# Kernel tuning notes

Hardware: AMD Instinct MI355X
Metric: run time of the kernel (lower is better)

## Reference

```python
import jax, jax.numpy as jnp
import numpy as np

RRELU_SLOPE = (1.0 / 8.0 + 1.0 / 3.0) / 2.0  # F.rrelu eval mode
N_ENT, N_REL2, H, E, B, T = 20000, 460, 128, 400000, 1024, 8


def _lin(x, W, b):
    return x @ W.T + b  # torch nn.Linear convention


def _gru_cell(x, h, w_ih, w_hh, b_ih, b_hh):
    gi = x @ w_ih.T + b_ih
    gh = h @ w_hh.T + b_hh
    i_r, i_z, i_n = jnp.split(gi, 3, axis=1)
    h_r, h_z, h_n = jnp.split(gh, 3, axis=1)
    r = jax.nn.sigmoid(i_r + h_r)
    z = jax.nn.sigmoid(i_z + h_z)
    n = jnp.tanh(i_n + r * h_n)
    return (1.0 - z) * n + z * h


def setup_inputs() -> dict:
    key = jax.random.key(0)
    ks = jax.random.split(key, 24)
    s = 0.02
    inp = {
        'ent_emb': jax.random.normal(ks[0], (N_ENT, H), jnp.float32),
        'rel_emb': jax.random.normal(ks[1], (N_REL2, H), jnp.float32),
        'weight_neighbor': jax.random.normal(ks[2], (H, H), jnp.float32) * s,
        'loop_weight': jax.random.normal(ks[3], (H, H), jnp.float32) * s,
        'evolve_loop_weight': jax.random.normal(ks[4], (H, H), jnp.float32) * s,
        'w_ih': jax.random.normal(ks[5], (3 * H, H), jnp.float32) * s,
        'w_hh': jax.random.normal(ks[6], (3 * H, H), jnp.float32) * s,
        'b_ih': jnp.zeros((3 * H,), jnp.float32),
        'b_hh': jnp.zeros((3 * H,), jnp.float32),
        'W_map1': jax.random.normal(ks[7], (2 * H, H), jnp.float32) * s,
        'b_map1': jnp.zeros((2 * H,), jnp.float32),
        'W_map2': jax.random.normal(ks[8], (H, 2 * H), jnp.float32) * s,
        'b_map2': jnp.zeros((H,), jnp.float32),
        'W_h1': jax.random.normal(ks[9], (H, H), jnp.float32) * s,
        'b_h1': jnp.zeros((H,), jnp.float32),
        'W_h2': jax.random.normal(ks[10], (H, H), jnp.float32) * s,
        'b_h2': jnp.zeros((H,), jnp.float32),
        'W_align': jax.random.normal(ks[11], (H, H), jnp.float32) * s,
        'b_align': jnp.zeros((H,), jnp.float32),
        'W_attn': jax.random.normal(ks[12], (H, H), jnp.float32) * s,
        'b_attn': jnp.zeros((H,), jnp.float32),
    }
    u = jax.random.uniform(ks[13], (B, T * N_REL2), jnp.float32)
    mask = jax.random.uniform(ks[14], (B, T * N_REL2)) > 0.7  # sparse history
    inp['partial_embeding'] = u * mask
    inp['edge_src'] = jax.random.randint(ks[15], (E,), 0, N_ENT, jnp.int32)
    inp['edge_dst'] = jax.random.randint(ks[16], (E,), 0, N_ENT, jnp.int32)
    inp['edge_type'] = jax.random.randint(ks[17], (E,), 0, N_REL2, jnp.int32)
    sub = jax.random.randint(ks[18], (B,), 0, N_ENT, jnp.int32)
    rel = jax.random.randint(ks[19], (B,), 0, N_REL2, jnp.int32)
    obj = jax.random.randint(ks[20], (B,), 0, N_ENT, jnp.int32)
    inp['triples'] = jnp.stack([sub, rel, obj], axis=1)
    return inp


def reference(ent_emb, rel_emb, weight_neighbor, loop_weight, evolve_loop_weight,
              w_ih, w_hh, b_ih, b_hh, W_map1, b_map1, W_map2, b_map2,
              W_h1, b_h1, W_h2, b_h2, W_align, b_align, W_attn, b_attn,
              partial_embeding, edge_src, edge_dst, edge_type, triples):
    # ---- UnionRGCNLayer: gather-transform-scatter ----
    h = ent_emb
    msg = (h[edge_src] + rel_emb[edge_type]) @ weight_neighbor          # [E, H]
    agg = jax.ops.segment_sum(msg, edge_dst, num_segments=N_ENT)        # [N, H]
    deg = jax.ops.segment_sum(jnp.ones((edge_dst.shape[0],), h.dtype), edge_dst,
                              num_segments=N_ENT)
    norm = jnp.where(deg > 0, 1.0 / jnp.where(deg > 0, deg, 1.0), 0.0)[:, None]
    loop = jnp.where((deg > 0)[:, None], h @ loop_weight, h @ evolve_loop_weight)
    x = agg * norm + loop
    pre_emb = jnp.where(x >= 0, x, x * RRELU_SLOPE)                     # rrelu (eval)

    # ---- PathPredictor.forward_back ----
    mapped_rel = _lin(_lin(rel_emb, W_map1, b_map1), W_map2, b_map2)    # [2R, H]
    q_rel = mapped_rel[triples[:, 1]]                                   # [B, H]
    A = _lin(q_rel, W_attn, b_attn) @ mapped_rel.T                      # [B, 2R]
    hist = partial_embeding.reshape(B, T, N_REL2).transpose(1, 0, 2)    # [T, B, 2R]

    def step(gh, cur):
        attn = cur * A
        attn = jax.nn.softmax(jnp.where(attn == 0, -1e9, attn), axis=1)
        rel_path = attn @ mapped_rel                                    # [B, H]
        return _gru_cell(rel_path, gh, w_ih, w_hh, b_ih, b_hh), None

    gru_hidden, _ = jax.lax.scan(step, jnp.zeros((B, H), pre_emb.dtype), hist)
    predicted_hist = 0.1 * _lin(_lin(q_rel, W_h1, b_h1), W_h2, b_h2) + q_rel
    match_loss = jnp.mean((predicted_hist - gru_hidden) ** 2)

    # ---- forward_forth, distmult scoring ----
    gh2 = _gru_cell(q_rel, predicted_hist, w_ih, w_hh, b_ih, b_hh)      # [B, H]
    sub_emb = pre_emb[triples[:, 0]]
    aligned_all = _lin(pre_emb, W_align, b_align)                       # [N, H]
    score_ = (_lin(sub_emb, W_align, b_align) * gh2) @ aligned_all.T    # [B, N]
    score = jax.nn.sigmoid(score_)
    # BCE(score, one_hot(obj)) without materializing labels:
    logp = jax.nn.log_sigmoid(score_)
    log1mp = jax.nn.log_sigmoid(-score_)
    total = -jnp.sum(log1mp)
    rows = jnp.arange(B)
    total = total + jnp.sum(log1mp[rows, triples[:, 2]] - logp[rows, triples[:, 2]])
    path_loss = total / (B * N_ENT)
    return score, match_loss, path_loss
```

## Files before the change

kernel.cpp:

```cpp
#include <hip/hip_runtime.h>

typedef unsigned short u16;
typedef unsigned int u32;
typedef __attribute__((ext_vector_type(8))) short bf8v;
typedef __attribute__((ext_vector_type(4))) float f4v;

#define RRELU_SLOPE 0.22916666667f

__device__ inline float bf2f(u16 u){ unsigned int i = ((unsigned int)u) << 16; float f; __builtin_memcpy(&f, &i, 4); return f; }
__device__ inline u16 f2bf(float f){ unsigned int i; __builtin_memcpy(&i, &f, 4); unsigned int r = (i + 0x7fffu + ((i >> 16) & 1u)) >> 16; return (u16)r; }
__device__ inline float frcp(float x){ return __builtin_amdgcn_rcpf(x); }
__device__ inline float fsigm(float x){ return frcp(1.f + __expf(-x)); }
__device__ inline float ftanh(float x){ return 2.f * frcp(1.f + __expf(-2.f * x)) - 1.f; }

__global__ __launch_bounds__(256) void prep_k(
    const float* __restrict__ Wn, const float* __restrict__ Wl, const float* __restrict__ We,
    const float* __restrict__ wih, const float* __restrict__ whh,
    const float* __restrict__ m1, const float* __restrict__ m2,
    const float* __restrict__ h1, const float* __restrict__ h2,
    const float* __restrict__ attn, const float* __restrict__ alg, const float* __restrict__ rel,
    const float* __restrict__ ent, const float* __restrict__ bat, const float* __restrict__ bh1,
    const float* __restrict__ bm1, const float* __restrict__ bm2,
    const int* __restrict__ edst, int E,
    u16* __restrict__ Bcat, u16* __restrict__ wihb, u16* __restrict__ whhb,
    u16* __restrict__ m1b, u16* __restrict__ m2b, u16* __restrict__ h1b, u16* __restrict__ h2b,
    u16* __restrict__ attnb, u16* __restrict__ algb, u16* __restrict__ relb,
    u16* __restrict__ entb, float* __restrict__ bias2,
    u16* __restrict__ wcb, float* __restrict__ bcombf, int* __restrict__ hist)
{
    int id = blockIdx.x * 256 + threadIdx.x;
    if (id < 49152) {
        int n = id / 384, k = id % 384;
        float v = (k < 128) ? Wn[k*128 + n] : (k < 256 ? Wl[(k-128)*128 + n] : We[(k-256)*128 + n]);
        Bcat[id] = f2bf(v); return;
    }
    id -= 49152;
    if (id < 49152) { wihb[id] = f2bf(wih[id]); return; } id -= 49152;
    if (id < 49152) { whhb[id] = f2bf(whh[id]); return; } id -= 49152;
    if (id < 32768) { m1b[id]  = f2bf(m1[id]);  return; } id -= 32768;
    if (id < 32768) { m2b[id]  = f2bf(m2[id]);  return; } id -= 32768;
    if (id < 16384) { h1b[id]  = f2bf(h1[id]);  return; } id -= 16384;
    if (id < 16384) { h2b[id]  = f2bf(h2[id]);  return; } id -= 16384;
    if (id < 16384) { attnb[id]= f2bf(attn[id]);return; } id -= 16384;
    if (id < 16384) { algb[id] = f2bf(alg[id]); return; } id -= 16384;
    if (id < 58880) { relb[id] = f2bf(rel[id]); return; } id -= 58880;
    if (id < 2560000) { entb[id] = f2bf(ent[id]); return; } id -= 2560000;
    if (id < 256) { bias2[id] = (id < 128) ? bat[id] : bh1[id - 128]; return; } id -= 256;
    if (id < 16384) {
        int n = id >> 7, j = id & 127;
        const float* w2r = m2 + n * 256;
        float s = 0.f;
        for (int k = 0; k < 256; ++k) s += w2r[k] * m1[k*128 + j];
        wcb[id] = f2bf(s); return;
    } id -= 16384;
    if (id < 128) {
        const float* w2r = m2 + id * 256;
        float s = bm2[id];
        for (int k = 0; k < 256; ++k) s += w2r[k] * bm1[k];
        bcombf[id] = s; return;
    } id -= 128;
    if (id < E) atomicAdd(&hist[edst[id]], 1);
}

__global__ __launch_bounds__(1024) void scan_k(
    const int* __restrict__ hist, int* __restrict__ starts, int* __restrict__ cursor)
{
    __shared__ int part[1024];
    int t = threadIdx.x;
    int base = t * 20;
    int s = 0;
    for (int j = 0; j < 20; ++j) { int idx = base + j; if (idx < 20000) s += hist[idx]; }
    part[t] = s;
    __syncthreads();
    for (int off = 1; off < 1024; off <<= 1) {
        int v = (t >= off) ? part[t - off] : 0;
        __syncthreads();
        part[t] += v;
        __syncthreads();
    }
    int run = (t > 0) ? part[t - 1] : 0;
    for (int j = 0; j < 20; ++j) {
        int idx = base + j;
        if (idx < 20000) { starts[idx] = run; cursor[idx] = run; run += hist[idx]; }
    }
    if (t == 1023) starts[20000] = run;
}

__global__ __launch_bounds__(256) void scmap_k(
    const int* __restrict__ src, const int* __restrict__ dst, const int* __restrict__ typ,
    int* __restrict__ cursor, int2* __restrict__ spack, int E, int eb,
    const u16* __restrict__ relb, const u16* __restrict__ wcb, const float* __restrict__ bcombf,
    u16* __restrict__ mapb, u16* __restrict__ mapT)
{
    int tid = threadIdx.x;
    if ((int)blockIdx.x < eb) {
        int e = blockIdx.x * 256 + tid;
        if (e >= E) return;
        int d = dst[e];
        int p = atomicAdd(&cursor[d], 1);
        spack[p] = make_int2(src[e], typ[e]);
        return;
    }
    int wave = tid >> 6, lane = tid & 63;
    int ln = lane & 15, q = lane >> 4;
    int base = (blockIdx.x - eb) * 64 + wave * 16;
    int arow = base + ln; if (arow > 459) arow = 459;
    const u16* Ap = relb + arow * 128;
    f4v acc[8] = {};
    for (int kc = 0; kc < 128; kc += 32) {
        bf8v af = *(const bf8v*)(Ap + kc + q*8);
#pragma unroll
        for (int nt = 0; nt < 8; ++nt) {
            bf8v bv = *(const bf8v*)(wcb + (nt*16 + ln)*128 + kc + q*8);
            acc[nt] = __builtin_amdgcn_mfma_f32_16x16x32_bf16(af, bv, acc[nt], 0, 0, 0);
        }
    }
#pragma unroll
    for (int nt = 0; nt < 8; ++nt) {
        int n = nt*16 + ln;
        float bv = bcombf[n];
#pragma unroll
        for (int r = 0; r < 4; ++r) {
            int m = base + q*4 + r;
            if (m < 460) {
                u16 hv = f2bf(acc[nt][r] + bv);
                mapb[m*128 + n] = hv;
                mapT[n*480 + m] = hv;
            }
        }
    }
}

__global__ __launch_bounds__(256) void agg_k(
    const int2* __restrict__ spack, const int* __restrict__ starts,
    const u32* __restrict__ hb, const u32* __restrict__ rb, u32* __restrict__ Acat32)
{
    int tid = threadIdx.x;
    int wave = tid >> 6, lane = tid & 63;
    int i = blockIdx.x * 4 + wave;
    int s0 = starts[i], s1 = starts[i + 1];
    float sx = 0.f, sy = 0.f;
    int e = s0;
    for (; e + 4 <= s1; e += 4) {
        int2 st0 = spack[e], st1 = spack[e+1], st2 = spack[e+2], st3 = spack[e+3];
        u32 a0 = hb[(long)st0.x * 64 + lane]; u32 r0 = rb[(long)st0.y * 64 + lane];
        u32 a1 = hb[(long)st1.x * 64 + lane]; u32 r1 = rb[(long)st1.y * 64 + lane];
        u32 a2 = hb[(long)st2.x * 64 + lane]; u32 r2 = rb[(long)st2.y * 64 + lane];
        u32 a3 = hb[(long)st3.x * 64 + lane]; u32 r3 = rb[(long)st3.y * 64 + lane];
        sx += bf2f((u16)(a0 & 0xffff)) + bf2f((u16)(r0 & 0xffff));
        sy += bf2f((u16)(a0 >> 16))    + bf2f((u16)(r0 >> 16));
        sx += bf2f((u16)(a1 & 0xffff)) + bf2f((u16)(r1 & 0xffff));
        sy += bf2f((u16)(a1 >> 16))    + bf2f((u16)(r1 >> 16));
        sx += bf2f((u16)(a2 & 0xffff)) + bf2f((u16)(r2 & 0xffff));
        sy += bf2f((u16)(a2 >> 16))    + bf2f((u16)(r2 >> 16));
        sx += bf2f((u16)(a3 & 0xffff)) + bf2f((u16)(r3 & 0xffff));
        sy += bf2f((u16)(a3 >> 16))    + bf2f((u16)(r3 >> 16));
    }
    for (; e < s1; ++e) {
        int2 st = spack[e];
        u32 a = hb[(long)st.x * 64 + lane];
        u32 r = rb[(long)st.y * 64 + lane];
        sx += bf2f((u16)(a & 0xffff)) + bf2f((u16)(r & 0xffff));
        sy += bf2f((u16)(a >> 16))    + bf2f((u16)(r >> 16));
    }
    bool has = s1 > s0;
    float nrm = has ? frcp((float)(s1 - s0)) : 0.f;
    u32 hv = hb[(long)i * 64 + lane];
    u32 agg = (u32)f2bf(sx * nrm) | ((u32)f2bf(sy * nrm) << 16);
    long o = (long)i * 192 + lane;
    Acat32[o]       = agg;
    Acat32[o + 64]  = has ? hv : 0u;
    Acat32[o + 128] = has ? 0u : hv;
}

__global__ __launch_bounds__(256) void prealnq_k(
    const u16* __restrict__ acat, const u16* __restrict__ bcat,
    const u16* __restrict__ alb, const float* __restrict__ bal,
    u16* __restrict__ preb, u16* __restrict__ alnb,
    const u16* __restrict__ mapb, const int* __restrict__ trip,
    const u16* __restrict__ atb, const float* __restrict__ bias2,
    const u16* __restrict__ h2b, const float* __restrict__ bh2,
    u16* __restrict__ atq, float* __restrict__ pred, u16* __restrict__ X)
{
    __shared__ u16 lds[4][16][136];
    int tid = threadIdx.x;
    int wave = tid >> 6, lane = tid & 63;
    int ln = lane & 15, q = lane >> 4;
    if (blockIdx.x < 313) {
        int bm = blockIdx.x * 64 + wave * 16;
        int am = bm + ln; if (am > 19999) am = 19999;
        const u16* Ap = acat + (long)am * 384;
        f4v acc[8] = {};
        for (int kc = 0; kc < 384; kc += 32) {
            bf8v af = *(const bf8v*)(Ap + kc + q*8);
#pragma unroll
            for (int nt = 0; nt < 8; ++nt) {
                bf8v bv = *(const bf8v*)(bcat + (nt*16 + ln)*384 + kc + q*8);
                acc[nt] = __builtin_amdgcn_mfma_f32_16x16x32_bf16(af, bv, acc[nt], 0, 0, 0);
            }
        }
#pragma unroll
        for (int nt = 0; nt < 8; ++nt) {
            int n = nt*16 + ln;
#pragma unroll
            for (int r = 0; r < 4; ++r) {
                int m = bm + q*4 + r;
                float v = acc[nt][r];
                v = (v >= 0.f) ? v : v * RRELU_SLOPE;
                u16 hv = f2bf(v);
                lds[wave][q*4 + r][n] = hv;
                if (m < 20000) preb[(long)m*128 + n] = hv;
            }
        }
        f4v acc2[8] = {};
        for (int kc = 0; kc < 128; kc += 32) {
            bf8v af = *(const bf8v*)&lds[wave][ln][kc + q*8];
#pragma unroll
            for (int nt = 0; nt < 8; ++nt) {
                bf8v bv = *(const bf8v*)(alb + (nt*16 + ln)*128 + kc + q*8);
                acc2[nt] = __builtin_amdgcn_mfma_f32_16x16x32_bf16(af, bv, acc2[nt], 0, 0, 0);
            }
        }
#pragma unroll
        for (int nt = 0; nt < 8; ++nt) {
            int n = nt*16 + ln;
            float bv = bal[n];
#pragma unroll
            for (int r = 0; r < 4; ++r) {
                int m = bm + q*4 + r;
                if (m < 20000) alnb[(long)m*128 + n] = f2bf(acc2[nt][r] + bv);
            }
        }
        return;
    }
    int base = (blockIdx.x - 313) * 64 + wave * 16;
    int ar = trip[(base + ln)*3 + 1];
    const u16* Ap = mapb + ar * 128;
    int rm_[4];
#pragma unroll
    for (int r = 0; r < 4; ++r) rm_[r] = trip[(base + q*4 + r)*3 + 1];
    f4v acc1[16] = {};
    for (int kc = 0; kc < 128; kc += 32) {
        bf8v af = *(const bf8v*)(Ap + kc + q*8);
#pragma unroll
        for (int nt = 0; nt < 16; ++nt) {
            bf8v bv = *(const bf8v*)(atb + (nt*16 + ln)*128 + kc + q*8);
            acc1[nt] = __builtin_amdgcn_mfma_f32_16x16x32_bf16(af, bv, acc1[nt], 0, 0, 0);
        }
    }
#pragma unroll
    for (int nt = 0; nt < 16; ++nt) {
        int n = nt*16 + ln;
        float bv = bias2[n];
#pragma unroll
        for (int r = 0; r < 4; ++r) {
            int m = base + q*4 + r;
            float x = acc1[nt][r] + bv;
            if (nt < 8) {
                atq[m*128 + n] = f2bf(x);
                X[(long)(8192 + m)*128 + n] = mapb[rm_[r]*128 + n];
            } else lds[wave][q*4 + r][n - 128] = f2bf(x);
        }
    }
    f4v acc2[8] = {};
    for (int kc = 0; kc < 128; kc += 32) {
        bf8v af = *(const bf8v*)&lds[wave][ln][kc + q*8];
#pragma unroll
        for (int nt = 0; nt < 8; ++nt) {
            bf8v bv = *(const bf8v*)(h2b + (nt*16 + ln)*128 + kc + q*8);
            acc2[nt] = __builtin_amdgcn_mfma_f32_16x16x32_bf16(af, bv, acc2[nt], 0, 0, 0);
        }
    }
#pragma unroll
    for (int nt = 0; nt < 8; ++nt) {
        int n = nt*16 + ln;
        float bv = bh2[n];
#pragma unroll
        for (int r = 0; r < 4; ++r) {
            int m = base + q*4 + r;
            pred[(long)m*128 + n] = 0.1f * (acc2[nt][r] + bv) + bf2f(mapb[rm_[r]*128 + n]);
        }
    }
}

__global__ __launch_bounds__(256) void smrp_k(
    const u16* __restrict__ atq, const u16* __restrict__ mapb,
    const float* __restrict__ part, const u16* __restrict__ mapT, u16* __restrict__ X)
{
    __shared__ u16 xls[32][488];
    __shared__ float asl[4][464];
    int tid = threadIdx.x;
    int wave = tid >> 6, lane = tid & 63;
    int ln = lane & 15, q = lane >> 4;
    int b0 = blockIdx.x * 4;
    {
        const u16* Ap = atq + (long)(b0 + (ln & 3)) * 128;
        bf8v af[4];
#pragma unroll
        for (int kc = 0; kc < 4; ++kc) af[kc] = *(const bf8v*)(Ap + kc*32 + q*8);
        for (int nt = wave; nt < 29; nt += 4) {
            int brow = nt*16 + ln; if (brow > 459) brow = 459;
            f4v acc = {};
#pragma unroll
            for (int kc = 0; kc < 4; ++kc) {
                bf8v bv = *(const bf8v*)(mapb + (long)brow*128 + kc*32 + q*8);
                acc = __builtin_amdgcn_mfma_f32_16x16x32_bf16(af[kc], bv, acc, 0, 0, 0);
            }
            if (q == 0) {
                int n = nt*16 + ln;
                if (n < 460) {
#pragma unroll
                    for (int r = 0; r < 4; ++r) asl[r][n] = acc[r];
                }
            }
        }
    }
    __syncthreads();
    for (int j = 0; j < 8; ++j) {
        int rl = wave*8 + j;
        int t = rl >> 2, db = rl & 3;
        const float* crow = part + (long)(b0 + db)*3680 + t*460;
        float v[8], e[8];
        float m = -1e30f;
#pragma unroll
        for (int i = 0; i < 8; ++i) {
            int r = i*64 + lane;
            if (r < 460) {
                float x = crow[r] * asl[db][r];
                x = (x == 0.f) ? -1e9f : x;
                v[i] = x; m = fmaxf(m, x);
            } else v[i] = -1e30f;
        }
#pragma unroll
        for (int off = 32; off; off >>= 1) m = fmaxf(m, __shfl_xor(m, off));
        float sum = 0.f;
#pragma unroll
        for (int i = 0; i < 8; ++i) {
            int r = i*64 + lane;
            e[i] = 0.f;
            if (r < 460) { e[i] = __expf(v[i] - m); sum += e[i]; }
        }
#pragma unroll
        for (int off = 32; off; off >>= 1) sum += __shfl_xor(sum, off);
        float inv = frcp(sum);
#pragma unroll
        for (int i = 0; i < 8; ++i) {
            int r = i*64 + lane;
            if (r < 460)      xls[rl][r] = f2bf(e[i] * inv);
            else if (r < 488) xls[rl][r] = 0;
        }
    }
    __syncthreads();
    f4v acc[2][2] = {};
    for (int kc = 0; kc < 480; kc += 32) {
        bf8v a[2], bfr[2];
#pragma unroll
        for (int mt = 0; mt < 2; ++mt)
            a[mt] = *(const bf8v*)&xls[mt*16 + ln][kc + q*8];
#pragma unroll
        for (int nt = 0; nt < 2; ++nt)
            bfr[nt] = *(const bf8v*)(mapT + (wave*32 + nt*16 + ln)*480 + kc + q*8);
#pragma unroll
        for (int mt = 0; mt < 2; ++mt)
#pragma unroll
            for (int nt = 0; nt < 2; ++nt)
                acc[mt][nt] = __builtin_amdgcn_mfma_f32_16x16x32_bf16(a[mt], bfr[nt], acc[mt][nt], 0, 0, 0);
    }
#pragma unroll
    for (int mt = 0; mt < 2; ++mt)
#pragma unroll
    for (int nt = 0; nt < 2; ++nt) {
        int n = wave*32 + nt*16 + ln;
#pragma unroll
        for (int r = 0; r < 4; ++r) {
            int rl = mt*16 + q*4 + r;
            long m = (long)(rl >> 2)*1024 + b0 + (rl & 3);
            X[m*128 + n] = f2bf(acc[mt][nt][r]);
        }
    }
}

__global__ __launch_bounds__(256, 1) void gru_k(
    const u16* __restrict__ X, const u16* __restrict__ wihb, const float* __restrict__ bih,
    const u16* __restrict__ whhb, const float* __restrict__ bhh,
    const float* __restrict__ pred,
    const u16* __restrict__ preb, const u16* __restrict__ alb, const float* __restrict__ bal,
    const u16* __restrict__ AL, const int* __restrict__ trip,
    u16* __restrict__ V, float* __restrict__ accp)
{
    __shared__ u16  hbf[16][136];
    __shared__ float hf [4][128];
    __shared__ float ghl[4][388];
    __shared__ float gil[4][388];
    __shared__ float sll[4][132];
    __shared__ float redm[4], redo[4];
    int tid = threadIdx.x;
    int wave = tid >> 6, lane = tid & 63;
    int ln = lane & 15, q = lane >> 4;
    int bb = blockIdx.x * 4;
    for (int i = tid; i < 16*136; i += 256) hbf[i/136][i%136] = 0;
    for (int i = tid; i < 4*128; i += 256) hf[i>>7][i&127] = 0.f;
    bf8v bfrag[6][4], wfrag[6][4];
#pragma unroll
    for (int nt = 0; nt < 6; ++nt)
#pragma unroll
        for (int kc = 0; kc < 4; ++kc) {
            bfrag[nt][kc] = *(const bf8v*)(whhb + (long)(wave*96 + nt*16 + ln)*128 + kc*32 + q*8);
            wfrag[nt][kc] = *(const bf8v*)(wihb + (long)(wave*96 + nt*16 + ln)*128 + kc*32 + q*8);
        }
    {
        const u16* Pp = preb + (long)trip[(bb + (ln & 3))*3 + 0] * 128;
        f4v sacc[2] = {};
#pragma unroll
        for (int kc = 0; kc < 4; ++kc) {
            bf8v pf = *(const bf8v*)(Pp + kc*32 + q*8);
#pragma unroll
            for (int nt = 0; nt < 2; ++nt) {
                bf8v bv = *(const bf8v*)(alb + (long)(wave*32 + nt*16 + ln)*128 + kc*32 + q*8);
                sacc[nt] = __builtin_amdgcn_mfma_f32_16x16x32_bf16(pf, bv, sacc[nt], 0, 0, 0);
            }
        }
        if (q == 0) {
#pragma unroll
            for (int nt = 0; nt < 2; ++nt) {
                int n = wave*32 + nt*16 + ln;
                float bv = bal[n];
#pragma unroll
                for (int r = 0; r < 4; ++r) sll[r][n] = sacc[nt][r] + bv;
            }
        }
    }
    int k = tid & 127;
    float cr = bih[k] + bhh[k];
    float cz = bih[128 + k] + bhh[128 + k];
    float bin_ = bih[256 + k], bhn = bhh[256 + k];
    __syncthreads();
    float msum = 0.f, osum = 0.f;
    for (int t = 0; t <= 8; ++t) {
        float pv[2];
#pragma unroll
        for (int it = 0; it < 2; ++it) {
            int m = it*2 + (tid >> 7);
            pv[it] = (t >= 7) ? pred[(long)(bb + m)*128 + k] : 0.f;
        }
        if (t == 8) {
#pragma unroll
            for (int it = 0; it < 2; ++it) {
                int m = it*2 + (tid >> 7);
                hf[m][k] = pv[it]; hbf[m][k] = f2bf(pv[it]);
            }
            __syncthreads();
        }
        long xr0 = (t < 8) ? ((long)t*1024 + bb) : (long)(8192 + bb);
        const u16* Xp = X + (xr0 + (ln & 3))*128;
        f4v gacc[6] = {};
        f4v acc[6] = {};
#pragma unroll
        for (int kc = 0; kc < 4; ++kc) {
            bf8v xf = *(const bf8v*)(Xp + kc*32 + q*8);
            bf8v af = *(const bf8v*)&hbf[ln][kc*32 + q*8];
#pragma unroll
            for (int nt = 0; nt < 6; ++nt) {
                gacc[nt] = __builtin_amdgcn_mfma_f32_16x16x32_bf16(xf, wfrag[nt][kc], gacc[nt], 0, 0, 0);
                acc[nt]  = __builtin_amdgcn_mfma_f32_16x16x32_bf16(af, bfrag[nt][kc], acc[nt],  0, 0, 0);
            }
        }
        if (q == 0) {
#pragma unroll
            for (int nt = 0; nt < 6; ++nt)
#pragma unroll
                for (int r = 0; r < 4; ++r) {
                    ghl[r][wave*96 + nt*16 + ln] = acc[nt][r];
                    gil[r][wave*96 + nt*16 + ln] = gacc[nt][r];
                }
        }
        __syncthreads();
#pragma unroll
        for (int it = 0; it < 2; ++it) {
            int m = it*2 + (tid >> 7);
            float rr = fsigm(gil[m][k] + ghl[m][k] + cr);
            float zz = fsigm(gil[m][128 + k] + ghl[m][128 + k] + cz);
            float nn = ftanh(gil[m][256 + k] + bin_ + rr * (ghl[m][256 + k] + bhn));
            float hn = (1.f - zz) * nn + zz * hf[m][k];
            if (t == 7) { float d = pv[it] - hn; msum += d*d; }
            if (t == 8) {
                u16 vb = f2bf(sll[m][k] * hn);
                V[(long)(bb + m)*128 + k] = vb;
                int obj = trip[(bb + m)*3 + 2];
                osum += bf2f(vb) * bf2f(AL[(long)obj*128 + k]);
            } else { hf[m][k] = hn; hbf[m][k] = f2bf(hn); }
        }
        __syncthreads();
    }
#pragma unroll
    for (int off = 32; off; off >>= 1) { msum += __shfl_down(msum, off); osum += __shfl_down(osum, off); }
    if (lane == 0) { redm[wave] = msum; redo[wave] = osum; }
    __syncthreads();
    if (tid == 0) {
        atomicAdd(accp + 0, redm[0] + redm[1] + redm[2] + redm[3]);
        atomicAdd(accp + 2, -(redo[0] + redo[1] + redo[2] + redo[3]));
    }
}

__global__ __launch_bounds__(512) void score_k(
    const u16* __restrict__ V, const u16* __restrict__ AL,
    float* __restrict__ out, float* __restrict__ sp_acc, int N)
{
    __shared__ float stage[8][1024];
    int tid = threadIdx.x;
    int wave = tid >> 6, lane = tid & 63;
    int ln = lane & 15, q = lane >> 4;
    int bm = blockIdx.x * 128 + (wave >> 2) * 64;
    int bn = blockIdx.y * 128 + (wave & 3) * 32;
    bool valid = bn < N;
    int br[2];
#pragma unroll
    for (int nt = 0; nt < 2; ++nt) { int n = bn + nt*16 + ln; br[nt] = (n < N) ? n : (N - 1); }
    f4v acc[4][2] = {};
    for (int kc = 0; kc < 128; kc += 32) {
        bf8v a[4], b[2];
#pragma unroll
        for (int mt = 0; mt < 4; ++mt)
            a[mt] = *(const bf8v*)(V + (long)(bm + mt*16 + ln)*128 + kc + q*8);
#pragma unroll
        for (int nt = 0; nt < 2; ++nt)
            b[nt] = *(const bf8v*)(AL + (long)br[nt]*128 + kc + q*8);
#pragma unroll
        for (int mt = 0; mt < 4; ++mt)
#pragma unroll
            for (int nt = 0; nt < 2; ++nt)
                acc[mt][nt] = __builtin_amdgcn_mfma_f32_16x16x32_bf16(a[mt], b[nt], acc[mt][nt], 0, 0, 0);
    }
    float lsum = 0.f;
    float* st = stage[wave];
#pragma unroll
    for (int half = 0; half < 2; ++half) {
#pragma unroll
        for (int mh = 0; mh < 2; ++mh) {
            int mt = half*2 + mh;
#pragma unroll
            for (int nt = 0; nt < 2; ++nt)
#pragma unroll
            for (int r = 0; r < 4; ++r) {
                float s = acc[mt][nt][r];
                float e = __expf(-fabsf(s));
                float d = 1.f + e;
                float inv = frcp(d);
                st[(mh*16 + q*4 + r)*32 + nt*16 + ln] = (s >= 0.f) ? inv : e * inv;
                lsum += fmaxf(s, 0.f) + __logf(d);
            }
        }
        if (valid) {
            int row0 = lane >> 3, c4 = (lane & 7) << 2;
#pragma unroll
            for (int i = 0; i < 4; ++i) {
                int row = i*8 + row0;
                f4v vv = *(const f4v*)&st[row*32 + c4];
                *(f4v*)&out[(long)(bm + half*32 + row)*N + bn + c4] = vv;
            }
        }
    }
    if (!valid) lsum = 0.f;
#pragma unroll
    for (int off = 32; off; off >>= 1) lsum += __shfl_xor(lsum, off);
    __shared__ float red[8];
    if (lane == 0) red[wave] = lsum;
    __syncthreads();
    if (tid == 0) {
        float tsum = 0.f;
#pragma unroll
        for (int w = 0; w < 8; ++w) tsum += red[w];
        atomicAdd(sp_acc, tsum);
    }
}

__global__ void final_k(const float* __restrict__ acc, float* __restrict__ out)
{
    out[20480000] = acc[0] / (1024.f * 128.f);
    out[20480001] = (acc[1] + acc[2]) / (1024.f * 20000.f);
}

extern "C" void kernel_launch(void* const* d_in, const int* in_sizes, int n_in,
                              void* d_out, int out_size, void* d_ws, size_t ws_size,
                              hipStream_t stream)
{
    const float* ent  = (const float*)d_in[0];
    const float* rel  = (const float*)d_in[1];
    const float* Wn   = (const float*)d_in[2];
    const float* Wl   = (const float*)d_in[3];
    const float* We   = (const float*)d_in[4];
    const float* wih  = (const float*)d_in[5];
    const float* whh  = (const float*)d_in[6];
    const float* b_ih = (const float*)d_in[7];
    const float* b_hh = (const float*)d_in[8];
    const float* Wm1  = (const float*)d_in[9];
    const float* bm1  = (const float*)d_in[10];
    const float* Wm2  = (const float*)d_in[11];
    const float* bm2  = (const float*)d_in[12];
    const float* Wh1  = (const float*)d_in[13];
    const float* bh1  = (const float*)d_in[14];
    const float* Wh2  = (const float*)d_in[15];
    const float* bh2  = (const float*)d_in[16];
    const float* Wal  = (const float*)d_in[17];
    const float* bal  = (const float*)d_in[18];
    const float* Wat  = (const float*)d_in[19];
    const float* bat  = (const float*)d_in[20];
    const float* part = (const float*)d_in[21];
    const int* esrc   = (const int*)d_in[22];
    const int* edst   = (const int*)d_in[23];
    const int* etyp   = (const int*)d_in[24];
    const int* trip   = (const int*)d_in[25];
    float* out = (float*)d_out;
    const int E = in_sizes[22];

    char* ws = (char*)d_ws;
    size_t off = 0;
    auto alloc = [&](size_t bytes) { size_t o = off; off = (off + bytes + 255) & ~(size_t)255; return o; };

    size_t o_acc   = alloc(256);
    size_t o_hist  = alloc(20000 * 4);
    size_t o_mapT  = alloc(128 * 480 * 2);
    size_t zend = off;
    size_t o_starts= alloc(20004 * 4);
    size_t o_cur   = alloc(20000 * 4);
    size_t o_spack = alloc((size_t)E * 8);
    size_t o_entb  = alloc((size_t)20000 * 128 * 2);
    size_t o_acat  = alloc((size_t)20000 * 384 * 2);
    size_t o_pre   = alloc((size_t)20000 * 128 * 2);
    size_t o_aln   = alloc((size_t)20000 * 128 * 2);
    size_t o_bcat  = alloc(128 * 384 * 2);
    size_t o_wih   = alloc(384 * 128 * 2);
    size_t o_whh   = alloc(384 * 128 * 2);
    size_t o_m1    = alloc(256 * 128 * 2);
    size_t o_m2    = alloc(128 * 256 * 2);
    size_t o_ath   = alloc(2 * 128 * 128 * 2);
    size_t o_h2    = alloc(128 * 128 * 2);
    size_t o_al    = alloc(128 * 128 * 2);
    size_t o_rel   = alloc(460 * 128 * 2);
    size_t o_map   = alloc(460 * 128 * 2);
    size_t o_wcb   = alloc(128 * 128 * 2);
    size_t o_bcf   = alloc(128 * 4);
    size_t o_atq   = alloc(1024 * 128 * 2);
    size_t o_b2    = alloc(256 * 4);
    size_t o_pred  = alloc(1024 * 128 * 4);
    size_t o_X     = alloc((size_t)9216 * 128 * 2);
    size_t o_V     = alloc(1024 * 128 * 2);

    float* accp  = (float*)(ws + o_acc);
    int* histp   = (int*)(ws + o_hist);
    u16* mapT    = (u16*)(ws + o_mapT);
    int* startsp = (int*)(ws + o_starts);
    int* curp    = (int*)(ws + o_cur);
    int2* spack  = (int2*)(ws + o_spack);
    u16* entb    = (u16*)(ws + o_entb);
    u16* acat    = (u16*)(ws + o_acat);
    u16* preb    = (u16*)(ws + o_pre);
    u16* alnb    = (u16*)(ws + o_aln);
    u16* bcat    = (u16*)(ws + o_bcat);
    u16* wihb    = (u16*)(ws + o_wih);
    u16* whhb    = (u16*)(ws + o_whh);
    u16* m1b     = (u16*)(ws + o_m1);
    u16* m2b     = (u16*)(ws + o_m2);
    u16* atb     = (u16*)(ws + o_ath);
    u16* h1b     = atb + 128 * 128;
    u16* h2b     = (u16*)(ws + o_h2);
    u16* alb     = (u16*)(ws + o_al);
    u16* relb    = (u16*)(ws + o_rel);
    u16* mapb    = (u16*)(ws + o_map);
    u16* wcb     = (u16*)(ws + o_wcb);
    float* bcombf= (float*)(ws + o_bcf);
    u16* atqb    = (u16*)(ws + o_atq);
    float* bias2 = (float*)(ws + o_b2);
    float* predf = (float*)(ws + o_pred);
    u16* Xb      = (u16*)(ws + o_X);
    u16* Vb      = (u16*)(ws + o_V);

    hipMemsetAsync(ws, 0, zend, stream);

    int ptot = 2914176 + E;
    prep_k<<<(ptot + 255) / 256, 256, 0, stream>>>(
        Wn, Wl, We, wih, whh, Wm1, Wm2, Wh1, Wh2, Wat, Wal, rel,
        ent, bat, bh1, bm1, bm2, edst, E,
        bcat, wihb, whhb, m1b, m2b, h1b, h2b, atb, alb, relb,
        entb, bias2, wcb, bcombf, histp);

    scan_k<<<1, 1024, 0, stream>>>(histp, startsp, curp);

    int eb = (E + 255) / 256;
    scmap_k<<<eb + 8, 256, 0, stream>>>(esrc, edst, etyp, curp, spack, E, eb,
                                        relb, wcb, bcombf, mapb, mapT);

    agg_k<<<5000, 256, 0, stream>>>(spack, startsp, (const u32*)entb, (const u32*)relb, (u32*)acat);

    prealnq_k<<<329, 256, 0, stream>>>(acat, bcat, alb, bal, preb, alnb,
                                       mapb, trip, atb, bias2, h2b, bh2, atqb, predf, Xb);

    smrp_k<<<256, 256, 0, stream>>>(atqb, mapb, part, mapT, Xb);

    gru_k<<<256, 256, 0, stream>>>(Xb, wihb, b_ih, whhb, b_hh, predf, preb, alb, bal, alnb, trip, Vb, accp);

    score_k<<<dim3(8, 157), 512, 0, stream>>>(Vb, alnb, out, accp + 1, 20000);

    final_k<<<1, 1, 0, stream>>>(accp, out);

    (void)in_sizes; (void)n_in; (void)out_size; (void)ws_size;
}
```

Measured before the change: 397.5 us.

## Rewrite score kernel as persistent grid-stride loop over small tiles without LDS staging

The score GEMM kernel changes from 128x128 tiles with 512 threads, staged through shared memory for vectorized stores, to a persistent 2048-block grid that walks 32x64 tiles. Each wave computes a 32x16 tile and writes sigmoid outputs straight from MFMA accumulators to global memory. The aim is better load balance across CUs and no LDS staging or shared-memory footprint. The cost is scalar, less coalesced 4-byte stores to the 80MB output and less operand reuse per wave, since A rows are reloaded for every tile.

```diff
diff --git a/kernel.cpp b/kernel.cpp
--- a/kernel.cpp
+++ b/kernel.cpp
@@ -502,76 +502,51 @@
     }
 }
 
-__global__ __launch_bounds__(512) void score_k(
+__global__ __launch_bounds__(256) void score_k(
     const u16* __restrict__ V, const u16* __restrict__ AL,
     float* __restrict__ out, float* __restrict__ sp_acc, int N)
 {
-    __shared__ float stage[8][1024];
+    const int NCT = 313;
+    const int TILES = 32 * NCT;
     int tid = threadIdx.x;
     int wave = tid >> 6, lane = tid & 63;
     int ln = lane & 15, q = lane >> 4;
-    int bm = blockIdx.x * 128 + (wave >> 2) * 64;
-    int bn = blockIdx.y * 128 + (wave & 3) * 32;
-    bool valid = bn < N;
-    int br[2];
-#pragma unroll
-    for (int nt = 0; nt < 2; ++nt) { int n = bn + nt*16 + ln; br[nt] = (n < N) ? n : (N - 1); }
-    f4v acc[4][2] = {};
-    for (int kc = 0; kc < 128; kc += 32) {
-        bf8v a[4], b[2];
-#pragma unroll
-        for (int mt = 0; mt < 4; ++mt)
-            a[mt] = *(const bf8v*)(V + (long)(bm + mt*16 + ln)*128 + kc + q*8);
-#pragma unroll
-        for (int nt = 0; nt < 2; ++nt)
-            b[nt] = *(const bf8v*)(AL + (long)br[nt]*128 + kc + q*8);
-#pragma unroll
-        for (int mt = 0; mt < 4; ++mt)
-#pragma unroll
-            for (int nt = 0; nt < 2; ++nt)
-                acc[mt][nt] = __builtin_amdgcn_mfma_f32_16x16x32_bf16(a[mt], b[nt], acc[mt][nt], 0, 0, 0);
-    }
     float lsum = 0.f;
-    float* st = stage[wave];
-#pragma unroll
-    for (int half = 0; half < 2; ++half) {
-#pragma unroll
-        for (int mh = 0; mh < 2; ++mh) {
-            int mt = half*2 + mh;
-#pragma unroll
-            for (int nt = 0; nt < 2; ++nt)
+    for (int t = blockIdx.x; t < TILES; t += gridDim.x) {
+        int bm = (t / NCT) * 32;
+        int bn = (t % NCT) * 64 + wave * 16;
+        bool valid = bn < N;
+        int brow = valid ? (bn + ln) : (N - 1);
+        f4v acc[2] = {};
+#pragma unroll
+        for (int kc = 0; kc < 128; kc += 32) {
+            bf8v b  = *(const bf8v*)(AL + (long)brow*128 + kc + q*8);
+            bf8v a0 = *(const bf8v*)(V + (long)(bm + ln)*128 + kc + q*8);
+            bf8v a1 = *(const bf8v*)(V + (long)(bm + 16 + ln)*128 + kc + q*8);
+            acc[0] = __builtin_amdgcn_mfma_f32_16x16x32_bf16(a0, b, acc[0], 0, 0, 0);
+            acc[1] = __builtin_amdgcn_mfma_f32_16x16x32_bf16(a1, b, acc[1], 0, 0, 0);
+        }
+        if (valid) {
+#pragma unroll
+            for (int mt = 0; mt < 2; ++mt)
 #pragma unroll
             for (int r = 0; r < 4; ++r) {
-                float s = acc[mt][nt][r];
+                float s = acc[mt][r];
                 float e = __expf(-fabsf(s));
                 float d = 1.f + e;
                 float inv = frcp(d);
-                st[(mh*16 + q*4 + r)*32 + nt*16 + ln] = (s >= 0.f) ? inv : e * inv;
+                int m = bm + mt*16 + q*4 + r;
+                out[(long)m*N + bn + ln] = (s >= 0.f) ? inv : e * inv;
                 lsum += fmaxf(s, 0.f) + __logf(d);
             }
         }
-        if (valid) {
-            int row0 = lane >> 3, c4 = (lane & 7) << 2;
-#pragma unroll
-            for (int i = 0; i < 4; ++i) {
-                int row = i*8 + row0;
-                f4v vv = *(const f4v*)&st[row*32 + c4];
-                *(f4v*)&out[(long)(bm + half*32 + row)*N + bn + c4] = vv;
-            }
-        }
-    }
-    if (!valid) lsum = 0.f;
+    }
 #pragma unroll
     for (int off = 32; off; off >>= 1) lsum += __shfl_xor(lsum, off);
-    __shared__ float red[8];
+    __shared__ float red[4];
     if (lane == 0) red[wave] = lsum;
     __syncthreads();
-    if (tid == 0) {
-        float tsum = 0.f;
-#pragma unroll
-        for (int w = 0; w < 8; ++w) tsum += red[w];
-        atomicAdd(sp_acc, tsum);
-    }
+    if (tid == 0) atomicAdd(sp_acc, red[0] + red[1] + red[2] + red[3]);
 }
 
 __global__ void final_k(const float* __restrict__ acc, float* __restrict__ out)
@@ -699,7 +674,7 @@
 
     gru_k<<<256, 256, 0, stream>>>(Xb, wihb, b_ih, whhb, b_hh, predf, preb, alb, bal, alnb, trip, Vb, accp);
 
-    score_k<<<dim3(8, 157), 512, 0, stream>>>(Vb, alnb, out, accp + 1, 20000);
+    score_k<<<2048, 256, 0, stream>>>(Vb, alnb, out, accp + 1, 20000);
 
     final_k<<<1, 1, 0, stream>>>(accp, out);
 
```

After: 413.8 us. 1.04x slower.
